# Performance work log

Measured on AMD Instinct MI355X. Metric: run time of the kernel, lower is better.

Reference implementation:

```python
import jax, jax.numpy as jnp
import numpy as np

B, L, ENC, DEC, ATT = 256, 196, 2048, 512, 512


def setup_inputs() -> dict:
    key = jax.random.key(0)
    ks = jax.random.split(key, 10)
    s = lambda d: 1.0 / np.sqrt(d)
    return {
        "x": jax.random.normal(ks[0], (B, L, ENC), dtype=jnp.float32),
        "h": jax.random.normal(ks[1], (B, DEC), dtype=jnp.float32),
        "W_enc": jax.random.uniform(ks[2], (ENC, ATT), jnp.float32, -s(ENC), s(ENC)),
        "b_enc": jax.random.uniform(ks[3], (ATT,), jnp.float32, -s(ENC), s(ENC)),
        "W_dec": jax.random.uniform(ks[4], (DEC, ATT), jnp.float32, -s(DEC), s(DEC)),
        "b_dec": jax.random.uniform(ks[5], (ATT,), jnp.float32, -s(DEC), s(DEC)),
        "W_full": jax.random.uniform(ks[6], (ATT, 1), jnp.float32, -s(ATT), s(ATT)),
        "b_full": jax.random.uniform(ks[7], (1,), jnp.float32, -s(ATT), s(ATT)),
        "W_beta": jax.random.uniform(ks[8], (DEC, 1), jnp.float32, -s(DEC), s(DEC)),
        "b_beta": jax.random.uniform(ks[9], (1,), jnp.float32, -s(DEC), s(DEC)),
    }


def reference(x, h, W_enc, b_enc, W_dec, b_dec, W_full, b_full, W_beta, b_beta):
    # x: [B, L, ENC], h: [B, DEC]
    att1 = jnp.einsum("blc,ca->bla", x, W_enc) + b_enc          # [B, L, ATT]
    att2 = h @ W_dec + b_dec                                     # [B, ATT]
    att = (jax.nn.relu(att1 + att2[:, None, :]) @ W_full)[..., 0] + b_full  # [B, L]
    alpha = jax.nn.softmax(att, axis=-1)                         # [B, L]
    z = jnp.einsum("bl,blc->bc", alpha, x)                       # [B, ENC]
    gate_beta = jax.nn.sigmoid(h @ W_beta + b_beta)              # [B, 1]
    return gate_beta * z, alpha
```

## Files before the change

kernel.cpp:

```cpp
#include <hip/hip_runtime.h>
#include <hip/hip_bf16.h>
#include <cstdint>

#define B_   256
#define L_   196
#define ENC_ 2048
#define DEC_ 512
#define ATT_ 512
#define M_TOT (B_*L_)

typedef short short8 __attribute__((ext_vector_type(8)));
typedef float f32x16 __attribute__((ext_vector_type(16)));

__device__ __forceinline__ unsigned short f2bf(float f) {
    union { float f; unsigned u; } v; v.f = f;
    unsigned u = v.u;
    return (unsigned short)((u + 0x7FFFu + ((u >> 16) & 1u)) >> 16);
}

__device__ __forceinline__ void gl_lds16(const void* g, void* l) {
    __builtin_amdgcn_global_load_lds((const __attribute__((address_space(1))) unsigned int*)g,
                                     (__attribute__((address_space(3))) unsigned int*)l,
                                     16, 0, 0);
}

__global__ void k_transpose(const float* __restrict__ W, unsigned short* __restrict__ WT) {
    __shared__ float S[32*33];
    const int k0 = blockIdx.x * 32, n0 = blockIdx.y * 32;
    const int t  = threadIdx.x;
    const int c31 = t & 31, q = t >> 5;
#pragma unroll
    for (int i = 0; i < 4; ++i) {
        int kl = q + i*8;
        S[c31*33 + kl] = W[(size_t)(k0+kl)*ATT_ + n0 + c31];
    }
    __syncthreads();
#pragma unroll
    for (int i = 0; i < 4; ++i) {
        int nn = q + i*8;
        WT[(size_t)(n0+nn)*ENC_ + k0 + c31] = f2bf(S[nn*33 + c31]);
    }
}

__global__ void k_prep2(const float* __restrict__ h, const float* __restrict__ Wdec,
                        const float* __restrict__ bdec, const float* __restrict__ benc,
                        const float* __restrict__ Wbeta, const float* __restrict__ bbeta,
                        float* __restrict__ att2c, float* __restrict__ gate) {
    const int b = blockIdx.x, t = threadIdx.x;
    __shared__ float hs[DEC_];
    __shared__ float pr[4];
    hs[t]       = h[(size_t)b*DEC_ + t];
    hs[t + 256] = h[(size_t)b*DEC_ + t + 256];
    __syncthreads();
    float a0 = 0.f, a1 = 0.f;
    for (int k = 0; k < DEC_; ++k) {
        float hk = hs[k];
        a0 = fmaf(hk, Wdec[(size_t)k*ATT_ + t],       a0);
        a1 = fmaf(hk, Wdec[(size_t)k*ATT_ + t + 256], a1);
    }
    att2c[(size_t)b*ATT_ + t]       = a0 + bdec[t]       + benc[t];
    att2c[(size_t)b*ATT_ + t + 256] = a1 + bdec[t + 256] + benc[t + 256];
    float p = hs[t]*Wbeta[t] + hs[t+256]*Wbeta[t+256];
#pragma unroll
    for (int mask = 32; mask; mask >>= 1) p += __shfl_xor(p, mask, 64);
    if ((t & 63) == 0) pr[t >> 6] = p;
    __syncthreads();
    if (t == 0) gate[b] = 1.f / (1.f + __expf(-(pr[0]+pr[1]+pr[2]+pr[3] + bbeta[0])));
}

__global__ __launch_bounds__(256, 2) void k_gemm(
        const float* __restrict__ x, const unsigned short* __restrict__ WT,
        const float* __restrict__ att2c, const float* __restrict__ Wfull,
        float* __restrict__ att) {
    __shared__ alignas(16) unsigned short Ab[2][64*32];
    __shared__ alignas(16) unsigned short Bb[2][512*32];
    __shared__ float att_ws[4][64];

    const int tid   = threadIdx.x;
    const int wave  = tid >> 6;
    const int lane  = tid & 63;
    const int lane31 = lane & 31;
    const int laneh  = lane >> 5;
    const int m0 = blockIdx.x * 64;

    f32x16 acc[2][4];
#pragma unroll
    for (int i = 0; i < 2; ++i)
#pragma unroll
        for (int j = 0; j < 4; ++j)
#pragma unroll
            for (int r = 0; r < 16; ++r) acc[i][j][r] = 0.f;

    int boff[8];
#pragma unroll
    for (int j = 0; j < 8; ++j) {
        int c  = (wave*8 + j)*64 + lane;
        int n  = c >> 2;
        int kc = (c & 3) ^ ((n >> 1) & 3);
        boff[j] = n*ENC_ + kc*8;
    }
    const int ar = tid >> 2, g = tid & 3;
    const int achunk = ar*4 + (g ^ ((ar >> 1) & 3));
    const float* xrow = x + (size_t)(m0 + ar)*ENC_ + g*8;

    float4 pa0, pb0, pa1, pb1;
#pragma unroll
    for (int j = 0; j < 8; ++j)
        gl_lds16(WT + boff[j], (void*)&Bb[0][(wave*8 + j)*512]);
    pa0 = *(const float4*)(xrow);
    pb0 = *(const float4*)(xrow + 4);
#pragma unroll
    for (int j = 0; j < 8; ++j)
        gl_lds16(WT + boff[j] + 32, (void*)&Bb[1][(wave*8 + j)*512]);
    pa1 = *(const float4*)(xrow + 32);
    pb1 = *(const float4*)(xrow + 36);
    {
        short8 w;
        w[0] = f2bf(pa0.x); w[1] = f2bf(pa0.y); w[2] = f2bf(pa0.z); w[3] = f2bf(pa0.w);
        w[4] = f2bf(pb0.x); w[5] = f2bf(pb0.y); w[6] = f2bf(pb0.z); w[7] = f2bf(pb0.w);
        *(short8*)&Ab[0][achunk*8] = w;
    }
    asm volatile("s_waitcnt vmcnt(10) lgkmcnt(0)\n\ts_barrier" ::: "memory");

#define GEMM_ITER(K, XW0, XW1, XR0, XR1)                                              \
{                                                                                     \
    const int cur = (K) & 1, nxt = cur ^ 1;                                           \
    if ((K) + 2 < 64) {                             \
        XW0 = *(const float4*)(xrow + ((K)+2)*32);                                    \
        XW1 = *(const float4*)(xrow + ((K)+2)*32 + 4);                                \
    }                                                                                 \
    short8 a[2][2], bf[2][4];                                                         \
    _Pragma("unroll") for (int ks = 0; ks < 2; ++ks) {                                \
        _Pragma("unroll") for (int mi = 0; mi < 2; ++mi) {                            \
            int m  = mi*32 + lane31;                                                  \
            int ch = m*4 + ((ks*2 + laneh) ^ ((m >> 1) & 3));                         \
            a[ks][mi] = *(const short8*)&Ab[cur][ch*8];                               \
        }                                                                             \
        _Pragma("unroll") for (int ni = 0; ni < 4; ++ni) {                            \
            int n  = wave*128 + ni*32 + lane31;                                       \
            int ch = n*4 + ((ks*2 + laneh) ^ ((n >> 1) & 3));                         \
            bf[ks][ni] = *(const short8*)&Bb[cur][ch*8];                              \
        }                                                                             \
    }                                                                                 \
           \
    asm volatile("s_waitcnt lgkmcnt(0)" ::: "memory");                                \
    if ((K) + 2 < 64) {                                                               \
        _Pragma("unroll") for (int j = 0; j < 8; ++j)                                 \
            gl_lds16(WT + boff[j] + ((K)+2)*32, (void*)&Bb[cur][(wave*8 + j)*512]);   \
    }                                                                                 \
    _Pragma("unroll") for (int ks = 0; ks < 2; ++ks)                                  \
        _Pragma("unroll") for (int mi = 0; mi < 2; ++mi)                              \
            _Pragma("unroll") for (int ni = 0; ni < 4; ++ni)                          \
                acc[mi][ni] = __builtin_amdgcn_mfma_f32_32x32x16_bf16(                \
                                  a[ks][mi], bf[ks][ni], acc[mi][ni], 0, 0, 0);       \
    if ((K) + 1 < 64) {               \
        short8 w;                                                                     \
        w[0] = f2bf(XR0.x); w[1] = f2bf(XR0.y); w[2] = f2bf(XR0.z); w[3] = f2bf(XR0.w);\
        w[4] = f2bf(XR1.x); w[5] = f2bf(XR1.y); w[6] = f2bf(XR1.z); w[7] = f2bf(XR1.w);\
        *(short8*)&Ab[nxt][achunk*8] = w;                                             \
    }                                                                                 \
    if ((K) < 62)                                                                     \
        asm volatile("s_waitcnt vmcnt(10) lgkmcnt(0)\n\ts_barrier" ::: "memory");     \
    else                                                                              \
        asm volatile("s_waitcnt vmcnt(0) lgkmcnt(0)\n\ts_barrier" ::: "memory");      \
}

    for (int K = 0; K < 64; K += 2) {
        GEMM_ITER(K,     pa0, pb0, pa1, pb1)
        GEMM_ITER(K + 1, pa1, pb1, pa0, pb0)
    }
#undef GEMM_ITER

    float* epi = (float*)&Bb[0][0];
    {
        const int b0i = m0 / L_;
        const int b1i = (m0 + 63) / L_;
        epi[tid]        = Wfull[tid];
        epi[256 + tid]  = Wfull[256 + tid];
        epi[512 + tid]  = att2c[(size_t)b0i*ATT_ + tid];
        epi[768 + tid]  = att2c[(size_t)b0i*ATT_ + 256 + tid];
        epi[1024 + tid] = att2c[(size_t)b1i*ATT_ + tid];
        epi[1280 + tid] = att2c[(size_t)b1i*ATT_ + 256 + tid];
    }
    __syncthreads();
    const int split = (m0 / L_ + 1) * L_;
#pragma unroll
    for (int mi = 0; mi < 2; ++mi) {
#pragma unroll
        for (int reg = 0; reg < 16; ++reg) {
            int r32  = (reg & 3) + 8*(reg >> 2) + 4*laneh;
            int mloc = mi*32 + r32;
            int off  = (m0 + mloc >= split) ? 1024 : 512;
            float v = 0.f;
#pragma unroll
            for (int ni = 0; ni < 4; ++ni) {
                int n = wave*128 + ni*32 + lane31;
                float tv = acc[mi][ni][reg] + epi[off + n];
                v = fmaf(fmaxf(tv, 0.f), epi[n], v);
            }
#pragma unroll
            for (int mask = 16; mask; mask >>= 1) v += __shfl_xor(v, mask, 64);
            if (lane31 == 0) att_ws[wave][mloc] = v;
        }
    }
    __syncthreads();
    if (tid < 64)
        att[m0 + tid] = att_ws[0][tid] + att_ws[1][tid] + att_ws[2][tid] + att_ws[3][tid];
}

__global__ __launch_bounds__(256) void k_softz(
        const float* __restrict__ att, const float* __restrict__ x,
        const float* __restrict__ gate, float* __restrict__ out) {
    const int b = (B_ - 1) - (int)blockIdx.x;
    const int s = blockIdx.y, t = threadIdx.x;
    __shared__ float sa[L_];
    __shared__ float red[8];
    const int wid = t >> 6, lane = t & 63;
    float v = (t < L_) ? att[b*L_ + t] : -1e30f;
    float m = v;
#pragma unroll
    for (int mask = 32; mask; mask >>= 1) m = fmaxf(m, __shfl_xor(m, mask, 64));
    if (lane == 0) red[wid] = m;
    __syncthreads();
    m = fmaxf(fmaxf(red[0], red[1]), fmaxf(red[2], red[3]));
    float e = (t < L_) ? __expf(v - m) : 0.f;
    float sum = e;
#pragma unroll
    for (int mask = 32; mask; mask >>= 1) sum += __shfl_xor(sum, mask, 64);
    if (lane == 0) red[4 + wid] = sum;
    __syncthreads();
    sum = red[4] + red[5] + red[6] + red[7];
    float alpha = e / sum;
    if (t < L_) {
        sa[t] = alpha;
        if (s == 0) out[(size_t)B_*ENC_ + (size_t)b*L_ + t] = alpha;
    }
    __syncthreads();
    const float* xb = x + (size_t)b*L_*ENC_ + s*1024 + t*4;
    float4 z = {0.f, 0.f, 0.f, 0.f};
    float4 u[7], w[7];
#pragma unroll
    for (int i = 0; i < 7; ++i) u[i] = *(const float4*)(xb + (size_t)i*ENC_);
    for (int l0 = 0; l0 < 183; l0 += 7) {
#pragma unroll
        for (int i = 0; i < 7; ++i)
            w[i] = *(const float4*)(xb + (size_t)(l0 + 7 + i)*ENC_);
#pragma unroll
        for (int i = 0; i < 7; ++i) {
            float a_ = sa[l0 + i];
            z.x = fmaf(a_, u[i].x, z.x); z.y = fmaf(a_, u[i].y, z.y);
            z.z = fmaf(a_, u[i].z, z.z); z.w = fmaf(a_, u[i].w, z.w);
        }
#pragma unroll
        for (int i = 0; i < 7; ++i) u[i] = w[i];
    }
#pragma unroll
    for (int i = 0; i < 7; ++i) {
        float a_ = sa[189 + i];
        z.x = fmaf(a_, u[i].x, z.x); z.y = fmaf(a_, u[i].y, z.y);
        z.z = fmaf(a_, u[i].z, z.z); z.w = fmaf(a_, u[i].w, z.w);
    }
    const float gt = gate[b];
    float4 o; o.x = gt*z.x; o.y = gt*z.y; o.z = gt*z.z; o.w = gt*z.w;
    *(float4*)(out + (size_t)b*ENC_ + s*1024 + t*4) = o;
}

extern "C" void kernel_launch(void* const* d_in, const int* in_sizes, int n_in,
                              void* d_out, int out_size, void* d_ws, size_t ws_size,
                              hipStream_t stream) {
    const float* x      = (const float*)d_in[0];
    const float* h      = (const float*)d_in[1];
    const float* W_enc  = (const float*)d_in[2];
    const float* b_enc  = (const float*)d_in[3];
    const float* W_dec  = (const float*)d_in[4];
    const float* b_dec  = (const float*)d_in[5];
    const float* W_full = (const float*)d_in[6];
    const float* W_beta = (const float*)d_in[8];
    const float* b_beta = (const float*)d_in[9];
    float* out = (float*)d_out;

    char* ws = (char*)d_ws;
    unsigned short* WT = (unsigned short*)ws;
    float* att2c  = (float*)(ws + 2*1024*1024);
    float* gate   = (float*)(ws + 2*1024*1024 + 512*1024);
    float* attbuf = (float*)(ws + 2*1024*1024 + 512*1024 + 1024);

    k_transpose<<<dim3(ENC_/32, ATT_/32), 256, 0, stream>>>(W_enc, WT);
    k_prep2   <<<B_, 256, 0, stream>>>(h, W_dec, b_dec, b_enc, W_beta, b_beta, att2c, gate);
    k_gemm    <<<M_TOT/64, 256, 0, stream>>>(x, WT, att2c, W_full, attbuf);
    k_softz   <<<dim3(B_, 2), 256, 0, stream>>>(attbuf, x, gate, out);
}
```

Measured before the change: 762.0 us.

## Shrink GEMM tile to 32 rows with 16-wide K steps for higher occupancy

The attention-score GEMM now uses 32-row M tiles and 16-element K steps with smaller LDS buffers, and launch bounds target 3 blocks per CU. The aim is more concurrent blocks to hide memory latency. In exchange, each block re-reads all of the weight tile, so weight traffic doubles, and there are twice as many barriers with fewer MFMAs between them. The decoder projection kernel also processes 4 batch rows per block so each W_dec load is reused.

```diff
diff --git a/kernel.cpp b/kernel.cpp
--- a/kernel.cpp
+++ b/kernel.cpp
@@ -18,6 +18,10 @@
     return (unsigned short)((u + 0x7FFFu + ((u >> 16) & 1u)) >> 16);
 }
 
+__device__ __forceinline__ unsigned pack2(float2 v) {
+    return (unsigned)f2bf(v.x) | ((unsigned)f2bf(v.y) << 16);
+}
+
 __device__ __forceinline__ void gl_lds16(const void* g, void* l) {
     __builtin_amdgcn_global_load_lds((const __attribute__((address_space(1))) unsigned int*)g,
                                      (__attribute__((address_space(3))) unsigned int*)l,
@@ -46,165 +50,151 @@
                         const float* __restrict__ bdec, const float* __restrict__ benc,
                         const float* __restrict__ Wbeta, const float* __restrict__ bbeta,
                         float* __restrict__ att2c, float* __restrict__ gate) {
-    const int b = blockIdx.x, t = threadIdx.x;
-    __shared__ float hs[DEC_];
-    __shared__ float pr[4];
-    hs[t]       = h[(size_t)b*DEC_ + t];
-    hs[t + 256] = h[(size_t)b*DEC_ + t + 256];
-    __syncthreads();
-    float a0 = 0.f, a1 = 0.f;
+    const int b0 = blockIdx.x * 4, t = threadIdx.x;
+    __shared__ float hs[4][DEC_];
+    __shared__ float pr[4][4];
+#pragma unroll
+    for (int i = 0; i < 4; ++i) {
+        hs[i][t]       = h[(size_t)(b0+i)*DEC_ + t];
+        hs[i][t + 256] = h[(size_t)(b0+i)*DEC_ + t + 256];
+    }
+    __syncthreads();
+    float a0[4] = {0.f,0.f,0.f,0.f}, a1[4] = {0.f,0.f,0.f,0.f};
     for (int k = 0; k < DEC_; ++k) {
-        float hk = hs[k];
-        a0 = fmaf(hk, Wdec[(size_t)k*ATT_ + t],       a0);
-        a1 = fmaf(hk, Wdec[(size_t)k*ATT_ + t + 256], a1);
-    }
-    att2c[(size_t)b*ATT_ + t]       = a0 + bdec[t]       + benc[t];
-    att2c[(size_t)b*ATT_ + t + 256] = a1 + bdec[t + 256] + benc[t + 256];
-    float p = hs[t]*Wbeta[t] + hs[t+256]*Wbeta[t+256];
-#pragma unroll
-    for (int mask = 32; mask; mask >>= 1) p += __shfl_xor(p, mask, 64);
-    if ((t & 63) == 0) pr[t >> 6] = p;
-    __syncthreads();
-    if (t == 0) gate[b] = 1.f / (1.f + __expf(-(pr[0]+pr[1]+pr[2]+pr[3] + bbeta[0])));
-}
-
-__global__ __launch_bounds__(256, 2) void k_gemm(
+        float w0 = Wdec[(size_t)k*ATT_ + t];
+        float w1 = Wdec[(size_t)k*ATT_ + t + 256];
+#pragma unroll
+        for (int i = 0; i < 4; ++i) {
+            a0[i] = fmaf(hs[i][k], w0, a0[i]);
+            a1[i] = fmaf(hs[i][k], w1, a1[i]);
+        }
+    }
+    const float bd0 = bdec[t] + benc[t], bd1 = bdec[t+256] + benc[t+256];
+#pragma unroll
+    for (int i = 0; i < 4; ++i) {
+        att2c[(size_t)(b0+i)*ATT_ + t]       = a0[i] + bd0;
+        att2c[(size_t)(b0+i)*ATT_ + t + 256] = a1[i] + bd1;
+    }
+    const int wid = t >> 6;
+    const float wb0 = Wbeta[t], wb1 = Wbeta[t+256];
+#pragma unroll
+    for (int i = 0; i < 4; ++i) {
+        float p = hs[i][t]*wb0 + hs[i][t+256]*wb1;
+#pragma unroll
+        for (int mask = 32; mask; mask >>= 1) p += __shfl_xor(p, mask, 64);
+        if ((t & 63) == 0) pr[i][wid] = p;
+    }
+    __syncthreads();
+    if (t < 4)
+        gate[b0+t] = 1.f / (1.f + __expf(-(pr[t][0]+pr[t][1]+pr[t][2]+pr[t][3] + bbeta[0])));
+}
+
+__global__ __launch_bounds__(256, 3) void k_gemm(
         const float* __restrict__ x, const unsigned short* __restrict__ WT,
         const float* __restrict__ att2c, const float* __restrict__ Wfull,
         float* __restrict__ att) {
-    __shared__ alignas(16) unsigned short Ab[2][64*32];
-    __shared__ alignas(16) unsigned short Bb[2][512*32];
-    __shared__ float att_ws[4][64];
+    __shared__ alignas(16) unsigned short Ab[2][512];
+    __shared__ alignas(16) unsigned short Bb[2][8192];
+    __shared__ float att_ws[4][32];
 
     const int tid   = threadIdx.x;
     const int wave  = tid >> 6;
     const int lane  = tid & 63;
     const int lane31 = lane & 31;
     const int laneh  = lane >> 5;
-    const int m0 = blockIdx.x * 64;
-
-    f32x16 acc[2][4];
-#pragma unroll
-    for (int i = 0; i < 2; ++i)
-#pragma unroll
-        for (int j = 0; j < 4; ++j)
-#pragma unroll
-            for (int r = 0; r < 16; ++r) acc[i][j][r] = 0.f;
-
-    int boff[8];
-#pragma unroll
-    for (int j = 0; j < 8; ++j) {
-        int c  = (wave*8 + j)*64 + lane;
-        int n  = c >> 2;
-        int kc = (c & 3) ^ ((n >> 1) & 3);
-        boff[j] = n*ENC_ + kc*8;
-    }
-    const int ar = tid >> 2, g = tid & 3;
-    const int achunk = ar*4 + (g ^ ((ar >> 1) & 3));
-    const float* xrow = x + (size_t)(m0 + ar)*ENC_ + g*8;
-
-    float4 pa0, pb0, pa1, pb1;
-#pragma unroll
-    for (int j = 0; j < 8; ++j)
-        gl_lds16(WT + boff[j], (void*)&Bb[0][(wave*8 + j)*512]);
-    pa0 = *(const float4*)(xrow);
-    pb0 = *(const float4*)(xrow + 4);
-#pragma unroll
-    for (int j = 0; j < 8; ++j)
-        gl_lds16(WT + boff[j] + 32, (void*)&Bb[1][(wave*8 + j)*512]);
-    pa1 = *(const float4*)(xrow + 32);
-    pb1 = *(const float4*)(xrow + 36);
+    const int m0 = blockIdx.x * 32;
+
+    f32x16 acc[4];
+#pragma unroll
+    for (int j = 0; j < 4; ++j)
+#pragma unroll
+        for (int r = 0; r < 16; ++r) acc[j][r] = 0.f;
+
+    int bsrc[4];
+#pragma unroll
+    for (int j = 0; j < 4; ++j) {
+        int p = (wave*4 + j)*64 + lane;
+        int n = p >> 1;
+        int hh = (p & 1) ^ ((n >> 2) & 1);
+        bsrc[j] = n*ENC_ + hh*8;
+    }
+    const int am = tid >> 3, ae = tid & 7, ah = ae >> 2;
+    const int awoff = am*32 + ((ah ^ ((am >> 2) & 1)) << 4) + (ae & 3)*4;
+    const float* xrow = x + (size_t)(m0 + am)*ENC_ + 2*ae;
+
+    const int aoff = lane31*32 + ((laneh ^ ((lane31 >> 2) & 1)) << 4);
+    int boffr[4];
+#pragma unroll
+    for (int ni = 0; ni < 4; ++ni) {
+        int n = wave*128 + ni*32 + lane31;
+        boffr[ni] = n*32 + ((laneh ^ ((n >> 2) & 1)) << 4);
+    }
+
+#pragma unroll
+    for (int j = 0; j < 4; ++j)
+        gl_lds16(WT + bsrc[j], (void*)&Bb[0][(wave*4 + j)*512]);
     {
-        short8 w;
-        w[0] = f2bf(pa0.x); w[1] = f2bf(pa0.y); w[2] = f2bf(pa0.z); w[3] = f2bf(pa0.w);
-        w[4] = f2bf(pb0.x); w[5] = f2bf(pb0.y); w[6] = f2bf(pb0.z); w[7] = f2bf(pb0.w);
-        *(short8*)&Ab[0][achunk*8] = w;
-    }
-    asm volatile("s_waitcnt vmcnt(10) lgkmcnt(0)\n\ts_barrier" ::: "memory");
-
-#define GEMM_ITER(K, XW0, XW1, XR0, XR1)                                              \
+        float2 p0 = *(const float2*)xrow;
+        *(unsigned*)((char*)&Ab[0][0] + awoff) = pack2(p0);
+    }
+    float2 pxA = *(const float2*)(xrow + 16);
+    float2 pxB;
+    __syncthreads();
+
+#define GITER(K, PXOLD, PXNEW)                                                        \
 {                                                                                     \
     const int cur = (K) & 1, nxt = cur ^ 1;                                           \
-    if ((K) + 2 < 64) {                             \
-        XW0 = *(const float4*)(xrow + ((K)+2)*32);                                    \
-        XW1 = *(const float4*)(xrow + ((K)+2)*32 + 4);                                \
+    if ((K) + 2 < 128)                                                                \
+        PXNEW = *(const float2*)(xrow + ((K)+2)*16);                                  \
+    if ((K) + 1 < 128) {                                                              \
+        _Pragma("unroll") for (int j = 0; j < 4; ++j)                                 \
+            gl_lds16(WT + bsrc[j] + ((K)+1)*16, (void*)&Bb[nxt][(wave*4 + j)*512]);   \
     }                                                                                 \
-    short8 a[2][2], bf[2][4];                                                         \
-    _Pragma("unroll") for (int ks = 0; ks < 2; ++ks) {                                \
-        _Pragma("unroll") for (int mi = 0; mi < 2; ++mi) {                            \
-            int m  = mi*32 + lane31;                                                  \
-            int ch = m*4 + ((ks*2 + laneh) ^ ((m >> 1) & 3));                         \
-            a[ks][mi] = *(const short8*)&Ab[cur][ch*8];                               \
-        }                                                                             \
-        _Pragma("unroll") for (int ni = 0; ni < 4; ++ni) {                            \
-            int n  = wave*128 + ni*32 + lane31;                                       \
-            int ch = n*4 + ((ks*2 + laneh) ^ ((n >> 1) & 3));                         \
-            bf[ks][ni] = *(const short8*)&Bb[cur][ch*8];                              \
-        }                                                                             \
-    }                                                                                 \
-           \
-    asm volatile("s_waitcnt lgkmcnt(0)" ::: "memory");                                \
-    if ((K) + 2 < 64) {                                                               \
-        _Pragma("unroll") for (int j = 0; j < 8; ++j)                                 \
-            gl_lds16(WT + boff[j] + ((K)+2)*32, (void*)&Bb[cur][(wave*8 + j)*512]);   \
-    }                                                                                 \
-    _Pragma("unroll") for (int ks = 0; ks < 2; ++ks)                                  \
-        _Pragma("unroll") for (int mi = 0; mi < 2; ++mi)                              \
-            _Pragma("unroll") for (int ni = 0; ni < 4; ++ni)                          \
-                acc[mi][ni] = __builtin_amdgcn_mfma_f32_32x32x16_bf16(                \
-                                  a[ks][mi], bf[ks][ni], acc[mi][ni], 0, 0, 0);       \
-    if ((K) + 1 < 64) {               \
-        short8 w;                                                                     \
-        w[0] = f2bf(XR0.x); w[1] = f2bf(XR0.y); w[2] = f2bf(XR0.z); w[3] = f2bf(XR0.w);\
-        w[4] = f2bf(XR1.x); w[5] = f2bf(XR1.y); w[6] = f2bf(XR1.z); w[7] = f2bf(XR1.w);\
-        *(short8*)&Ab[nxt][achunk*8] = w;                                             \
-    }                                                                                 \
-    if ((K) < 62)                                                                     \
-        asm volatile("s_waitcnt vmcnt(10) lgkmcnt(0)\n\ts_barrier" ::: "memory");     \
-    else                                                                              \
-        asm volatile("s_waitcnt vmcnt(0) lgkmcnt(0)\n\ts_barrier" ::: "memory");      \
-}
-
-    for (int K = 0; K < 64; K += 2) {
-        GEMM_ITER(K,     pa0, pb0, pa1, pb1)
-        GEMM_ITER(K + 1, pa1, pb1, pa0, pb0)
-    }
-#undef GEMM_ITER
+    short8 afr, bfr[4];                                                               \
+    afr = *(const short8*)((const char*)&Ab[cur][0] + aoff);                          \
+    _Pragma("unroll") for (int ni = 0; ni < 4; ++ni)                                  \
+        bfr[ni] = *(const short8*)((const char*)&Bb[cur][0] + boffr[ni]);             \
+    _Pragma("unroll") for (int ni = 0; ni < 4; ++ni)                                  \
+        acc[ni] = __builtin_amdgcn_mfma_f32_32x32x16_bf16(afr, bfr[ni], acc[ni], 0, 0, 0); \
+    if ((K) + 1 < 128)                                                                \
+        *(unsigned*)((char*)&Ab[nxt][0] + awoff) = pack2(PXOLD);                      \
+    __syncthreads();                                                                  \
+}
+
+    for (int KK = 0; KK < 64; ++KK) {
+        GITER(2*KK,     pxA, pxB)
+        GITER(2*KK + 1, pxB, pxA)
+    }
+#undef GITER
 
     float* epi = (float*)&Bb[0][0];
-    {
-        const int b0i = m0 / L_;
-        const int b1i = (m0 + 63) / L_;
-        epi[tid]        = Wfull[tid];
-        epi[256 + tid]  = Wfull[256 + tid];
-        epi[512 + tid]  = att2c[(size_t)b0i*ATT_ + tid];
-        epi[768 + tid]  = att2c[(size_t)b0i*ATT_ + 256 + tid];
-        epi[1024 + tid] = att2c[(size_t)b1i*ATT_ + tid];
-        epi[1280 + tid] = att2c[(size_t)b1i*ATT_ + 256 + tid];
-    }
-    __syncthreads();
-    const int split = (m0 / L_ + 1) * L_;
-#pragma unroll
-    for (int mi = 0; mi < 2; ++mi) {
-#pragma unroll
-        for (int reg = 0; reg < 16; ++reg) {
-            int r32  = (reg & 3) + 8*(reg >> 2) + 4*laneh;
-            int mloc = mi*32 + r32;
-            int off  = (m0 + mloc >= split) ? 1024 : 512;
-            float v = 0.f;
-#pragma unroll
-            for (int ni = 0; ni < 4; ++ni) {
-                int n = wave*128 + ni*32 + lane31;
-                float tv = acc[mi][ni][reg] + epi[off + n];
-                v = fmaf(fmaxf(tv, 0.f), epi[n], v);
-            }
-#pragma unroll
-            for (int mask = 16; mask; mask >>= 1) v += __shfl_xor(v, mask, 64);
-            if (lane31 == 0) att_ws[wave][mloc] = v;
+    const int b0i = m0 / L_;
+    const int b1i = (m0 + 31) / L_;
+    epi[tid]        = Wfull[tid];
+    epi[256 + tid]  = Wfull[256 + tid];
+    epi[512 + tid]  = att2c[(size_t)b0i*ATT_ + tid];
+    epi[768 + tid]  = att2c[(size_t)b0i*ATT_ + 256 + tid];
+    epi[1024 + tid] = att2c[(size_t)b1i*ATT_ + tid];
+    epi[1280 + tid] = att2c[(size_t)b1i*ATT_ + 256 + tid];
+    __syncthreads();
+    const int split = (b0i + 1) * L_;
+#pragma unroll
+    for (int reg = 0; reg < 16; ++reg) {
+        int r32 = (reg & 3) + 8*(reg >> 2) + 4*laneh;
+        int off = (m0 + r32 >= split) ? 1024 : 512;
+        float v = 0.f;
+#pragma unroll
+        for (int ni = 0; ni < 4; ++ni) {
+            int n = wave*128 + ni*32 + lane31;
+            float tv = acc[ni][reg] + epi[off + n];
+            v = fmaf(fmaxf(tv, 0.f), epi[n], v);
         }
-    }
-    __syncthreads();
-    if (tid < 64)
+#pragma unroll
+        for (int mask = 16; mask; mask >>= 1) v += __shfl_xor(v, mask, 64);
+        if (lane31 == 0) att_ws[wave][r32] = v;
+    }
+    __syncthreads();
+    if (tid < 32)
         att[m0 + tid] = att_ws[0][tid] + att_ws[1][tid] + att_ws[2][tid] + att_ws[3][tid];
 }
 
@@ -286,7 +276,7 @@
     float* attbuf = (float*)(ws + 2*1024*1024 + 512*1024 + 1024);
 
     k_transpose<<<dim3(ENC_/32, ATT_/32), 256, 0, stream>>>(W_enc, WT);
-    k_prep2   <<<B_, 256, 0, stream>>>(h, W_dec, b_dec, b_enc, W_beta, b_beta, att2c, gate);
-    k_gemm    <<<M_TOT/64, 256, 0, stream>>>(x, WT, att2c, W_full, attbuf);
+    k_prep2   <<<B_/4, 256, 0, stream>>>(h, W_dec, b_dec, b_enc, W_beta, b_beta, att2c, gate);
+    k_gemm    <<<M_TOT/32, 256, 0, stream>>>(x, WT, att2c, W_full, attbuf);
     k_softz   <<<dim3(B_, 2), 256, 0, stream>>>(attbuf, x, gate, out);
 }
```

Result: slower. 1.099 ms (+44.2%).
